# Optimization experiments

Measured on AMD Instinct MI355X. Metric: run time of the kernel, lower is better.

## Reference

```python
import jax, jax.numpy as jnp
import numpy as np

B, C, H, W = 4, 256, 64, 64
CQK = C // 2


def setup_inputs() -> dict:
    key = jax.random.key(0)
    ks = jax.random.split(key, 8)
    s = 0.05
    return {
        "x": jax.random.normal(ks[0], (B, C, H, W), dtype=jnp.float32),
        "wq": jax.random.normal(ks[1], (CQK, C), dtype=jnp.float32) * s,
        "bq": jax.random.normal(ks[2], (CQK,), dtype=jnp.float32) * s,
        "wk": jax.random.normal(ks[3], (CQK, C), dtype=jnp.float32) * s,
        "bk": jax.random.normal(ks[4], (CQK,), dtype=jnp.float32) * s,
        "wv": jax.random.normal(ks[5], (C, C), dtype=jnp.float32) * s,
        "bv": jax.random.normal(ks[6], (C,), dtype=jnp.float32) * s,
        "gamma": jax.random.normal(ks[7], (1,), dtype=jnp.float32),
    }


def reference(x, wq, bq, wk, bk, wv, bv, gamma):
    b, c, h, w = x.shape
    n = h * w
    xf = x.reshape(b, c, n)  # [B,C,N]
    # 1x1 convs == per-pixel linear projections
    q = jnp.einsum("oc,bcn->bon", wq, xf) + bq[:, None]  # [B,C/2,N]
    k = jnp.einsum("oc,bcn->bon", wk, xf) + bk[:, None]  # [B,C/2,N]
    v = jnp.einsum("oc,bcn->bon", wv, xf) + bv[:, None]  # [B,C,N]
    # attention[b,m,n'] = softmax_n'( sum_d q[b,d,m] * k[b,d,n'] )
    scores = jnp.einsum("bdm,bdn->bmn", q, k)  # [B,N,N]
    attn = jax.nn.softmax(scores, axis=2)
    # out_feat[b,c,j] = sum_i v[b,c,i] * attn[b,i,j]  (matmul(value, attention))
    af = jnp.einsum("bci,bij->bcj", v, attn)  # [B,C,N]
    out = gamma[0] * af.reshape(b, c, h, w) + x
    return out
```

## Files before the change

kernel.cpp:

```cpp
#include <hip/hip_runtime.h>
#include <hip/hip_bf16.h>


typedef _Float16 f16;
typedef _Float16 f16x4v __attribute__((ext_vector_type(4)));
typedef _Float16 f16x8v __attribute__((ext_vector_type(8)));
typedef float f32x4v __attribute__((ext_vector_type(4)));

static __device__ __forceinline__ f32x4v mfma16(f16x8v a, f16x8v b, f32x4v c) {
  return __builtin_amdgcn_mfma_f32_16x16x32_f16(a, b, c, 0, 0, 0);
}

#define AS1q __attribute__((address_space(1)))
#define AS3q __attribute__((address_space(3)))
static __device__ __forceinline__ void gl_lds16(const void* g, void* l) {
  __builtin_amdgcn_global_load_lds((const AS1q unsigned int*)g,
                                   (AS3q unsigned int*)l, 16, 0, 0);
}

__global__ void k_wcvt(const float* __restrict__ wq, const float* __restrict__ bq,
                       const float* __restrict__ wk, const float* __restrict__ bk,
                       const float* __restrict__ wv, const float* __restrict__ bv,
                       f16* __restrict__ wh, float* __restrict__ bcat) {
  int o = blockIdx.x;
  int c = threadIdx.x;
  const float* wrow; float bias;
  if (o < 128)      { wrow = wq + (size_t)o * 256;         bias = bq[o]; }
  else if (o < 256) { wrow = wk + (size_t)(o - 128) * 256; bias = bk[o - 128]; }
  else              { wrow = wv + (size_t)(o - 256) * 256; bias = bv[o - 256]; }
  wh[(size_t)o * 256 + c] = (f16)wrow[c];
  if (c == 0) bcat[o] = bias;
}

__global__ void k_xsplit(const float* __restrict__ x, f16* __restrict__ xh) {
  __shared__ float t[64][65];
  int b = blockIdx.z, c0 = blockIdx.y * 64, n0 = blockIdx.x * 64;
  int tx = threadIdx.x & 63, ty = threadIdx.x >> 6;
  const float* xb = x + ((size_t)b * 256 + c0) * 4096 + n0;
#pragma unroll
  for (int r = ty; r < 64; r += 4) t[r][tx] = xb[(size_t)r * 4096 + tx];
  __syncthreads();
  f16* dh = xh + ((size_t)b * 4096 + n0) * 256 + c0;
#pragma unroll
  for (int r = ty; r < 64; r += 4)
    dh[(size_t)r * 256 + tx] = (f16)t[tx][r];
}

__global__ void __launch_bounds__(256, 2)
k_proj(const f16* __restrict__ xh, const f16* __restrict__ wh,
       const float* __restrict__ bcat, f16* __restrict__ qT,
       f16* __restrict__ kT, f16* __restrict__ vT) {
  extern __shared__ char smem[];
  int b = blockIdx.z, m0 = blockIdx.y * 64, n0 = blockIdx.x * 64;
  int tid = threadIdx.x, l = tid & 63, w = tid >> 6;
  int col = l & 15, quad = l >> 4;
  const f16* Ag = xh + ((size_t)b * 4096 + m0) * 256;
  const f16* Wg = wh + (size_t)n0 * 256;
  int rloc = l >> 5;
  int l5 = l & 31;
#pragma unroll
  for (int p = 0; p < 8; p++) {
    int ci = w * 8 + p;
    int r = ci * 2 + rloc;
    int g = l5 ^ (r & 31);
    gl_lds16(Ag + (size_t)r * 256 + g * 8, smem + ci * 1024);
    gl_lds16(Wg + (size_t)r * 256 + g * 8, smem + 32768 + ci * 1024);
  }
  __syncthreads();
  const char* sA = smem;
  const char* sW = smem + 32768;
  f32x4v acc[4] = {};
  int ar = w * 16 + col;
#pragma unroll
  for (int ks = 0; ks < 8; ks++) {
    int G = ks * 4 + quad;
    f16x8v a = *(const f16x8v*)(sA + ar * 512 + ((G ^ (ar & 31)) * 16));
#pragma unroll
    for (int nt = 0; nt < 4; nt++) {
      int wr = nt * 16 + col;
      f16x8v bb = *(const f16x8v*)(sW + wr * 512 + ((G ^ (wr & 31)) * 16));
      acc[nt] = mfma16(a, bb, acc[nt]);
    }
  }
  if (n0 < 256) {
#pragma unroll
    for (int nt = 0; nt < 4; nt++) {
      int o = n0 + nt * 16 + col;
      float bias = bcat[o];
      int d = o & 127;
      f16* dst = (o < 128) ? qT : kT;
      size_t tb = (size_t)b * 524288 + (size_t)(m0 / 16 + w) * 2048 +
                  (size_t)(d >> 5) * 512 + (size_t)((d >> 3) & 3) * 128 + (d & 7);
#pragma unroll
      for (int rg = 0; rg < 4; rg++)
        dst[tb + (quad * 4 + rg) * 8] = (f16)(acc[nt][rg] + bias);
    }
  } else {
    int i2 = w * 16 + quad * 4;
    int it2 = (m0 + i2) >> 5;
    int qd2 = (i2 >> 3) & 3;
    int e2 = i2 & 7;
#pragma unroll
    for (int nt = 0; nt < 4; nt++) {
      int o = n0 + nt * 16 + col;
      float bias = bcat[o];
      int c = o - 256;
      f16x4v pv;
#pragma unroll
      for (int rg = 0; rg < 4; rg++) pv[rg] = (f16)(acc[nt][rg] + bias);
      size_t addr = (size_t)b * 1048576 + (size_t)(c >> 4) * 65536 +
                    (size_t)it2 * 512 + (size_t)qd2 * 128 + (size_t)(c & 15) * 8 + e2;
      *(f16x4v*)&vT[addr] = pv;
    }
  }
}

__global__ void __launch_bounds__(512, 2)
k_rows(const f16* __restrict__ qT, const f16* __restrict__ kT,
       float* __restrict__ partial) {
  int jblk = blockIdx.x, ih = blockIdx.y, b = blockIdx.z;
  int tid = threadIdx.x, l = tid & 63, w = tid >> 6;
  int col = l & 15;
  int ti = w & 3, half = w >> 2, tjb = half * 2;
  const f16* ktb = kT + (size_t)b * 524288 + (size_t)(jblk * 4 + tjb) * 2048 + l * 8;
  const f16* qtb = qT + (size_t)b * 524288 + (size_t)ti * 2048 + l * 8;
  f16x8v ka0[4], ka1[4];
#pragma unroll
  for (int ks = 0; ks < 4; ks++) {
    ka0[ks] = *(const f16x8v*)(ktb + ks * 512);
    ka1[ks] = *(const f16x8v*)(ktb + 2048 + ks * 512);
  }
  float* pout = partial + ((size_t)(b * 64 + jblk) * 2 + half) * 4096 + ti * 16 + col;
  int it0 = ih * 32;
  f16x8v qfA[4], qfB[4];
#pragma unroll
  for (int ks = 0; ks < 4; ks++)
    qfA[ks] = *(const f16x8v*)(qtb + (size_t)it0 * 8192 + ks * 512);

#define ROWS_BODY(IT, QF, QN, PREF)                                           \
  {                                                                           \
    if (PREF) {                                                               \
      _Pragma("unroll") for (int ks = 0; ks < 4; ks++)                        \
        QN[ks] = *(const f16x8v*)(qtb + (size_t)((IT) + 1) * 8192 + ks * 512);\
    }                                                                         \
    f32x4v s0 = {}, s1 = {};                                                  \
    _Pragma("unroll") for (int ks = 0; ks < 4; ks++) {                        \
      s0 = mfma16(ka0[ks], QF[ks], s0);                                       \
      s1 = mfma16(ka1[ks], QF[ks], s1);                                       \
    }                                                                         \
    float t = 0.f;                                                            \
    _Pragma("unroll") for (int rg = 0; rg < 4; rg++)                          \
      t += __expf(s0[rg]) + __expf(s1[rg]);                                   \
    t += __shfl_xor(t, 16);                                                   \
    t += __shfl_xor(t, 32);                                                   \
    if (l < 16) pout[(size_t)(IT) * 64] = t;                                  \
  }

  for (int itp = 0; itp < 16; itp++) {
    int itA = it0 + itp * 2;
    ROWS_BODY(itA, qfA, qfB, true)
    ROWS_BODY(itA + 1, qfB, qfA, itp < 15)
  }
#undef ROWS_BODY
}

__global__ void k_rsum(const float* __restrict__ partial, float* __restrict__ rinv) {
  int b = blockIdx.y;
  int i = blockIdx.x * 256 + threadIdx.x;
  const float* p = partial + (size_t)b * 128 * 4096 + i;
  float s = 0.f;
#pragma unroll 8
  for (int jb = 0; jb < 128; jb++) s += p[(size_t)jb * 4096];
  rinv[(size_t)b * 4096 + i] = 1.0f / s;
}

__global__ void __launch_bounds__(512, 2)
k_fav(const f16* __restrict__ qT, const f16* __restrict__ kT,
      const f16* __restrict__ vT, const float* __restrict__ rinv,
      const float* __restrict__ x, const float* __restrict__ gamma,
      float* __restrict__ out) {
  __shared__ f16 sE[2][4096];
  int wg = blockIdx.x;
  int lg = (wg & 7) * 32 + (wg >> 3);
  int b = lg >> 6, j0 = (lg & 63) * 64;
  int tid = threadIdx.x, l = tid & 63, w = tid >> 6;
  int col = l & 15, quad = l >> 4;
  int ti = w & 3, tjb = (w >> 2) * 2;
  const f16* ktb = kT + (size_t)b * 524288 + (size_t)(j0 / 16 + tjb) * 2048 + l * 8;
  const f16* qtb = qT + (size_t)b * 524288 + (size_t)ti * 2048 + l * 8;
  const f16* vtb = vT + (size_t)b * 1048576 + (size_t)(w * 2) * 65536 + l * 8;
  const float* rp = rinv + (size_t)b * 4096 + ti * 16 + col;
  f16x8v ka0[4], ka1[4];
#pragma unroll
  for (int ks = 0; ks < 4; ks++) {
    ka0[ks] = *(const f16x8v*)(ktb + ks * 512);
    ka1[ks] = *(const f16x8v*)(ktb + 2048 + ks * 512);
  }
  f16x8v qfA[4], qfB[4], vfA[2][2], vfB[2][2];
  float rvA, rvB;
#pragma unroll
  for (int ks = 0; ks < 4; ks++) qfA[ks] = *(const f16x8v*)(qtb + ks * 512);
#pragma unroll
  for (int mt = 0; mt < 2; mt++)
#pragma unroll
    for (int ks = 0; ks < 2; ks++)
      vfA[mt][ks] = *(const f16x8v*)(vtb + mt * 65536 + ks * 512);
  rvA = rp[0];
  f32x4v acc[2][4] = {};
  int ig = ti * 2 + (col >> 3);
  int i_lo = col & 7;

#define FAV_BODY(IT, QF, VF, RV, QN, VN, RN, PREF, SEB)                        \
  {                                                                            \
    if (PREF) {                                                                \
      _Pragma("unroll") for (int ks = 0; ks < 4; ks++)                         \
        QN[ks] = *(const f16x8v*)(qtb + (size_t)((IT) + 1) * 8192 + ks * 512); \
      _Pragma("unroll") for (int mt = 0; mt < 2; mt++)                         \
        _Pragma("unroll") for (int ks = 0; ks < 2; ks++)                       \
          VN[mt][ks] = *(const f16x8v*)(vtb + mt * 65536 +                     \
                                        (size_t)(((IT) + 1) * 2 + ks) * 512);  \
      RN = rp[((IT) + 1) * 64];                                                \
    }                                                                          \
    f32x4v s0 = {}, s1 = {};                                                   \
    _Pragma("unroll") for (int ks = 0; ks < 4; ks++) {                         \
      s0 = mfma16(ka0[ks], QF[ks], s0);                                        \
      s1 = mfma16(ka1[ks], QF[ks], s1);                                        \
    }                                                                          \
    _Pragma("unroll") for (int rg = 0; rg < 4; rg++) {                         \
      int jl0 = tjb * 16 + quad * 4 + rg;                                      \
      sE[SEB][jl0 * 64 + ((ig ^ (jl0 & 7)) * 8) + i_lo] = (f16)(__expf(s0[rg]) * RV); \
      sE[SEB][(jl0 + 16) * 64 + ((ig ^ (jl0 & 7)) * 8) + i_lo] = (f16)(__expf(s1[rg]) * RV); \
    }                                                                          \
    asm volatile("s_waitcnt lgkmcnt(0)\n\ts_barrier" ::: "memory");            \
    _Pragma("unroll") for (int ks = 0; ks < 2; ks++) {                         \
      int sw = ((ks * 4 + quad) ^ (col & 7)) * 8;                              \
      f16x8v e0 = *(const f16x8v*)&sE[SEB][col * 64 + sw];                     \
      f16x8v e1 = *(const f16x8v*)&sE[SEB][(16 + col) * 64 + sw];              \
      f16x8v e2 = *(const f16x8v*)&sE[SEB][(32 + col) * 64 + sw];              \
      f16x8v e3 = *(const f16x8v*)&sE[SEB][(48 + col) * 64 + sw];              \
      acc[0][0] = mfma16(VF[0][ks], e0, acc[0][0]);                            \
      acc[0][1] = mfma16(VF[0][ks], e1, acc[0][1]);                            \
      acc[0][2] = mfma16(VF[0][ks], e2, acc[0][2]);                            \
      acc[0][3] = mfma16(VF[0][ks], e3, acc[0][3]);                            \
      acc[1][0] = mfma16(VF[1][ks], e0, acc[1][0]);                            \
      acc[1][1] = mfma16(VF[1][ks], e1, acc[1][1]);                            \
      acc[1][2] = mfma16(VF[1][ks], e2, acc[1][2]);                            \
      acc[1][3] = mfma16(VF[1][ks], e3, acc[1][3]);                            \
    }                                                                          \
  }

  for (int itp = 0; itp < 32; itp++) {
    int itA = itp * 2;
    FAV_BODY(itA, qfA, vfA, rvA, qfB, vfB, rvB, true, 0)
    FAV_BODY(itA + 1, qfB, vfB, rvB, qfA, vfA, rvA, itp < 31, 1)
  }
#undef FAV_BODY

  float gm = gamma[0];
  const float* xb = x + (size_t)b * 256 * 4096;
  float* ob = out + (size_t)b * 256 * 4096;
#pragma unroll
  for (int mt = 0; mt < 2; mt++)
#pragma unroll
    for (int jt = 0; jt < 4; jt++) {
      int c = w * 32 + mt * 16 + quad * 4;
      int j = j0 + jt * 16 + col;
#pragma unroll
      for (int rg = 0; rg < 4; rg++) {
        size_t off = (size_t)(c + rg) * 4096 + j;
        ob[off] = gm * acc[mt][jt][rg] + xb[off];
      }
    }
}

extern "C" void kernel_launch(void* const* d_in, const int* in_sizes, int n_in,
                              void* d_out, int out_size, void* d_ws, size_t ws_size,
                              hipStream_t stream) {
  (void)in_sizes; (void)n_in; (void)out_size; (void)ws_size;
  const float* x  = (const float*)d_in[0];
  const float* wq = (const float*)d_in[1];
  const float* bq = (const float*)d_in[2];
  const float* wk = (const float*)d_in[3];
  const float* bk = (const float*)d_in[4];
  const float* wv = (const float*)d_in[5];
  const float* bv = (const float*)d_in[6];
  const float* gm = (const float*)d_in[7];
  float* out = (float*)d_out;

  char* ws = (char*)d_ws;
  f16*  xh = (f16*)ws;
  f16*  qT = (f16*)(ws + 8388608);
  f16*  kT = (f16*)(ws + 12582912);
  f16*  vT = (f16*)(ws + 16777216);
  f16*  wh = (f16*)(ws + 25165824);
  float* bcat    = (float*)(ws + 25427968);
  float* rinv    = (float*)(ws + 25430016);
  float* partial = (float*)(ws + 25495552);

  hipLaunchKernelGGL(k_wcvt, dim3(512), dim3(256), 0, stream, wq, bq, wk, bk, wv, bv, wh, bcat);
  hipLaunchKernelGGL(k_xsplit, dim3(64, 4, 4), dim3(256), 0, stream, x, xh);
  hipLaunchKernelGGL(k_proj, dim3(8, 64, 4), dim3(256), 65536, stream, xh, wh, bcat, qT, kT, vT);
  hipLaunchKernelGGL(k_rows, dim3(64, 2, 4), dim3(512), 0, stream, qT, kT, partial);
  hipLaunchKernelGGL(k_rsum, dim3(16, 4), dim3(256), 0, stream, partial, rinv);
  hipLaunchKernelGGL(k_fav, dim3(256), dim3(512), 0, stream, qT, kT, vT, rinv, x, gm, out);
}
```

Before: 191.1 us.

## Software-pipeline score MFMAs one tile ahead and pack exp writes to LDS

```diff
diff --git a/kernel.cpp b/kernel.cpp
--- a/kernel.cpp
+++ b/kernel.cpp
@@ -6,9 +6,16 @@
 typedef _Float16 f16x4v __attribute__((ext_vector_type(4)));
 typedef _Float16 f16x8v __attribute__((ext_vector_type(8)));
 typedef float f32x4v __attribute__((ext_vector_type(4)));
+typedef unsigned int u32;
 
 static __device__ __forceinline__ f32x4v mfma16(f16x8v a, f16x8v b, f32x4v c) {
   return __builtin_amdgcn_mfma_f32_16x16x32_f16(a, b, c, 0, 0, 0);
+}
+
+static __device__ __forceinline__ u32 pk2(float a, float b) {
+  union { f16 h[2]; u32 u; } cv;
+  cv.h[0] = (f16)a; cv.h[1] = (f16)b;
+  return cv.u;
 }
 
 #define AS1q __attribute__((address_space(1)))
@@ -189,7 +196,7 @@
   const f16* ktb = kT + (size_t)b * 524288 + (size_t)(j0 / 16 + tjb) * 2048 + l * 8;
   const f16* qtb = qT + (size_t)b * 524288 + (size_t)ti * 2048 + l * 8;
   const f16* vtb = vT + (size_t)b * 1048576 + (size_t)(w * 2) * 65536 + l * 8;
-  const float* rp = rinv + (size_t)b * 4096 + ti * 16 + col;
+  const float* rp = rinv + (size_t)b * 4096 + ti * 16 + quad * 4;
   f16x8v ka0[4], ka1[4];
 #pragma unroll
   for (int ks = 0; ks < 4; ks++) {
@@ -197,41 +204,59 @@
     ka1[ks] = *(const f16x8v*)(ktb + 2048 + ks * 512);
   }
   f16x8v qfA[4], qfB[4], vfA[2][2], vfB[2][2];
-  float rvA, rvB;
+  f32x4v scA[2], scB[2], rvA, rvB;
 #pragma unroll
   for (int ks = 0; ks < 4; ks++) qfA[ks] = *(const f16x8v*)(qtb + ks * 512);
+  scA[0] = (f32x4v){}; scA[1] = (f32x4v){};
+#pragma unroll
+  for (int ks = 0; ks < 4; ks++) {
+    scA[0] = mfma16(qfA[ks], ka0[ks], scA[0]);
+    scA[1] = mfma16(qfA[ks], ka1[ks], scA[1]);
+  }
+#pragma unroll
+  for (int ks = 0; ks < 4; ks++)
+    qfB[ks] = *(const f16x8v*)(qtb + 8192 + ks * 512);
 #pragma unroll
   for (int mt = 0; mt < 2; mt++)
 #pragma unroll
     for (int ks = 0; ks < 2; ks++)
       vfA[mt][ks] = *(const f16x8v*)(vtb + mt * 65536 + ks * 512);
-  rvA = rp[0];
+  rvA = *(const f32x4v*)rp;
   f32x4v acc[2][4] = {};
-  int ig = ti * 2 + (col >> 3);
-  int i_lo = col & 7;
-
-#define FAV_BODY(IT, QF, VF, RV, QN, VN, RN, PREF, SEB)                        \
+  int jr0 = tjb * 16 + col;
+  int swz = (((ti * 2 + (quad >> 1)) ^ (col & 7)) * 8) + (quad & 1) * 4;
+
+#define FAV_IT(IT, SC, SN, QKF, QPF, VF, VN, RV, RN, SEB)                      \
   {                                                                            \
-    if (PREF) {                                                                \
+             \
+    u32 w00 = pk2(__expf(SC[0][0]) * RV[0], __expf(SC[0][1]) * RV[1]);         \
+    u32 w01 = pk2(__expf(SC[0][2]) * RV[2], __expf(SC[0][3]) * RV[3]);         \
+    u32 w10 = pk2(__expf(SC[1][0]) * RV[0], __expf(SC[1][1]) * RV[1]);         \
+    u32 w11 = pk2(__expf(SC[1][2]) * RV[2], __expf(SC[1][3]) * RV[3]);         \
+    *(u32*)&sE[SEB][jr0 * 64 + swz] = w00;                                     \
+    *(u32*)&sE[SEB][jr0 * 64 + swz + 2] = w01;                                 \
+    *(u32*)&sE[SEB][(jr0 + 16) * 64 + swz] = w10;                              \
+    *(u32*)&sE[SEB][(jr0 + 16) * 64 + swz + 2] = w11;                          \
+             \
+    {                                                                          \
+      int qit = (IT) + 2 > 63 ? 63 : (IT) + 2;                                 \
+      int vit = (IT) + 1 > 63 ? 63 : (IT) + 1;                                 \
       _Pragma("unroll") for (int ks = 0; ks < 4; ks++)                         \
-        QN[ks] = *(const f16x8v*)(qtb + (size_t)((IT) + 1) * 8192 + ks * 512); \
+        QPF[ks] = *(const f16x8v*)(qtb + (size_t)qit * 8192 + ks * 512);       \
       _Pragma("unroll") for (int mt = 0; mt < 2; mt++)                         \
         _Pragma("unroll") for (int ks = 0; ks < 2; ks++)                       \
           VN[mt][ks] = *(const f16x8v*)(vtb + mt * 65536 +                     \
-                                        (size_t)(((IT) + 1) * 2 + ks) * 512);  \
-      RN = rp[((IT) + 1) * 64];                                                \
+                                        (size_t)(vit * 2 + ks) * 512);         \
+      RN = *(const f32x4v*)(rp + (size_t)vit * 64);                            \
     }                                                                          \
-    f32x4v s0 = {}, s1 = {};                                                   \
+                         \
+    SN[0] = (f32x4v){}; SN[1] = (f32x4v){};                                    \
     _Pragma("unroll") for (int ks = 0; ks < 4; ks++) {                         \
-      s0 = mfma16(ka0[ks], QF[ks], s0);                                        \
-      s1 = mfma16(ka1[ks], QF[ks], s1);                                        \
-    }                                                                          \
-    _Pragma("unroll") for (int rg = 0; rg < 4; rg++) {                         \
-      int jl0 = tjb * 16 + quad * 4 + rg;                                      \
-      sE[SEB][jl0 * 64 + ((ig ^ (jl0 & 7)) * 8) + i_lo] = (f16)(__expf(s0[rg]) * RV); \
-      sE[SEB][(jl0 + 16) * 64 + ((ig ^ (jl0 & 7)) * 8) + i_lo] = (f16)(__expf(s1[rg]) * RV); \
+      SN[0] = mfma16(QKF[ks], ka0[ks], SN[0]);                                 \
+      SN[1] = mfma16(QKF[ks], ka1[ks], SN[1]);                                 \
     }                                                                          \
     asm volatile("s_waitcnt lgkmcnt(0)\n\ts_barrier" ::: "memory");            \
+                                                           \
     _Pragma("unroll") for (int ks = 0; ks < 2; ks++) {                         \
       int sw = ((ks * 4 + quad) ^ (col & 7)) * 8;                              \
       f16x8v e0 = *(const f16x8v*)&sE[SEB][col * 64 + sw];                     \
@@ -251,10 +276,10 @@
 
   for (int itp = 0; itp < 32; itp++) {
     int itA = itp * 2;
-    FAV_BODY(itA, qfA, vfA, rvA, qfB, vfB, rvB, true, 0)
-    FAV_BODY(itA + 1, qfB, vfB, rvB, qfA, vfA, rvA, itp < 31, 1)
-  }
-#undef FAV_BODY
+    FAV_IT(itA,     scA, scB, qfB, qfA, vfA, vfB, rvA, rvB, 0)
+    FAV_IT(itA + 1, scB, scA, qfA, qfB, vfB, vfA, rvB, rvA, 1)
+  }
+#undef FAV_IT
 
   float gm = gamma[0];
   const float* xb = x + (size_t)b * 256 * 4096;
```

After: 197.0 us. 3.1% more time.
